# Kernel tuning notes

Hardware: AMD Instinct MI355X
Metric: run time of the kernel (lower is better)

Reference implementation:

```python
import jax, jax.numpy as jnp
import numpy as np

B, N, C = 2, 120000, 80
K = 300            # fixed NMS candidate pad per class (>> expected ~150 above threshold)
MAX_DET = 100      # max_detections_per_images
SCORE_THRES = 0.99875
NMS_THRES = 0.5
MIN_SIZE = 1e-3    # remove_small_boxes min_size
BBOX_CLIP = float(np.log(1000.0 / 16.0))  # standard decode clamp on dw, dh


def _decode(deltas, anchors):
    # activ_2_bbox: standard anchor-delta decode (xyxy anchors)
    wa = anchors[:, 2] - anchors[:, 0]
    ha = anchors[:, 3] - anchors[:, 1]
    cxa = anchors[:, 0] + 0.5 * wa
    cya = anchors[:, 1] + 0.5 * ha
    dx, dy = deltas[:, 0], deltas[:, 1]
    dw = jnp.minimum(deltas[:, 2], BBOX_CLIP)
    dh = jnp.minimum(deltas[:, 3], BBOX_CLIP)
    cx = dx * wa + cxa
    cy = dy * ha + cya
    w = jnp.exp(dw) * wa
    h = jnp.exp(dh) * ha
    return jnp.stack([cx - 0.5 * w, cy - 0.5 * h, cx + 0.5 * w, cy + 0.5 * h], axis=-1)


def _pairwise_iou(b):
    area = (b[:, 2] - b[:, 0]) * (b[:, 3] - b[:, 1])
    lt = jnp.maximum(b[:, None, :2], b[None, :, :2])
    rb = jnp.minimum(b[:, None, 2:], b[None, :, 2:])
    wh = jnp.clip(rb - lt, 0.0)
    inter = wh[..., 0] * wh[..., 1]
    return inter / (area[:, None] + area[None, :] - inter + 1e-9)


def _nms_keep(boxes, valid):
    # boxes sorted by descending score; greedy suppression over K candidates
    iou = jax.lax.stop_gradient(_pairwise_iou(boxes))  # masks only -> no grad path
    idx = jnp.arange(boxes.shape[0])
    def body(keep, i):
        suppress = keep[i] & (iou[i] > NMS_THRES) & (idx > i)
        return keep & ~suppress, None
    keep, _ = jax.lax.scan(body, valid, idx)
    return keep


def _per_image(box_pred, cls_pred, anchors, H, W):
    boxes = _decode(box_pred, anchors)
    boxes = jnp.stack([
        jnp.clip(boxes[:, 0], 0.0, W), jnp.clip(boxes[:, 1], 0.0, H),
        jnp.clip(boxes[:, 2], 0.0, W), jnp.clip(boxes[:, 3], 0.0, H)], axis=-1)
    big = ((boxes[:, 2] - boxes[:, 0]) >= MIN_SIZE) & ((boxes[:, 3] - boxes[:, 1]) >= MIN_SIZE)

    def class_step(valid, c):
        # faithful to the original: the validity set carries over across classes
        sc = cls_pred[:, c]
        v = valid & big & (sc > SCORE_THRES)
        ms = jnp.where(v, sc, -jnp.inf)
        sk, idx = jax.lax.top_k(ms, K)            # sorted desc, fixed-size pad
        vk = sk > -jnp.inf
        bk = boxes[idx]                            # [K,4]
        keep = _nms_keep(bk, vk)
        keep = keep & ((jnp.cumsum(keep) - 1) < MAX_DET)  # keep[:max_det]
        new_valid = jnp.zeros_like(valid).at[idx].set(keep)
        bk = jnp.where(keep[:, None], bk, 0.0)
        sk = jnp.where(keep, sk, 0.0)
        return new_valid, (bk, sk, keep)

    _, (bks, sks, keeps) = jax.lax.scan(class_step, jnp.ones(boxes.shape[0], bool), jnp.arange(C))
    out5 = jnp.concatenate([bks, sks[..., None]], axis=-1).reshape(C * K, 5)
    labels = jnp.broadcast_to(jnp.arange(C, dtype=jnp.int32)[:, None], (C, K)).reshape(C * K)
    return out5, labels, keeps.reshape(C * K)


def setup_inputs() -> dict:
    key = jax.random.key(0)
    k1, k2, k3, k4, k5 = jax.random.split(key, 5)
    H, W = 800, 1216
    box_preds = 0.2 * jax.random.normal(k1, (B, N, 4), jnp.float32)
    cls_preds = jax.random.uniform(k2, (B, N, C), dtype=jnp.float32)
    cx = jax.random.uniform(k3, (N,), dtype=jnp.float32) * W
    cy = jax.random.uniform(k4, (N,), dtype=jnp.float32) * H
    wh = 16.0 + 240.0 * jax.random.uniform(k5, (N, 2), dtype=jnp.float32)
    anchors = jnp.stack([cx - 0.5 * wh[:, 0], cy - 0.5 * wh[:, 1],
                         cx + 0.5 * wh[:, 0], cy + 0.5 * wh[:, 1]], axis=-1)
    return {"box_preds": box_preds, "cls_preds": cls_preds, "anchors": anchors,
            "image_h": H, "image_w": W}


def reference(box_preds, cls_preds, anchors, image_h, image_w):
    H = jnp.float32(image_h)
    W = jnp.float32(image_w)
    out5, labels, keep = jax.vmap(lambda bp, cp: _per_image(bp, cp, anchors, H, W))(box_preds, cls_preds)
    # out5: [B, C*K, 5] (x1,y1,x2,y2,score), zero-padded where keep is False
    return out5, labels, keep
```

## Files before the change

kernel.cpp:

```cpp
#include <hip/hip_runtime.h>
#include <stdint.h>

#define B_ 2
#define N_ 120000
#define C_ 80
#define K_ 300
#define MAXDET 100
#define CAP 1024
#define KTOP 300
#define NW 5

__device__ __constant__ float SCORE_THRES_F = 0.99875f;
__device__ __constant__ float NMS_THRES_F   = 0.5f;
__device__ __constant__ float MIN_SIZE_F    = 0.001f;
__device__ __constant__ float BBOX_CLIP_F   = 4.135166556742356f;

__global__ __launch_bounds__(256) void filter_init(
    const float* __restrict__ boxp, const float* __restrict__ clsp,
    const float* __restrict__ anch, const int* __restrict__ ih,
    const int* __restrict__ iw, int* __restrict__ counters,
    int* __restrict__ g_idx, float* __restrict__ g_sc,
    float4* __restrict__ g_bx, float* __restrict__ out) {
#pragma clang fp contract(off)
    const int NT  = gridDim.x * blockDim.x;
    const int tid = blockIdx.x * blockDim.x + threadIdx.x;

    const int CK  = C_ * K_;
    const int L0  = B_ * CK * 5;
    const int L1  = L0 + B_ * CK;
    const int TOT = L1 + B_ * CK;
    for (int i = tid; i < TOT; i += NT) {
        float v = 0.f;
        if (i >= L0 && i < L1) { int r = i - L0; v = (float)((r % CK) / K_); }
        out[i] = v;
    }

    const int BN = B_ * N_;
    float s[4]; int t4[4];
#pragma unroll
    for (int k = 0; k < 4; ++k) {
        int t = tid + k * NT;
        t4[k] = t;
        s[k] = (t < BN) ? clsp[(size_t)t * C_] : 0.f;
    }
#pragma unroll
    for (int k = 0; k < 4; ++k) {
        int t = t4[k];
        if (t < BN && s[k] > SCORE_THRES_F) {
            int b = t / N_, n = t - b * N_;
            float W = (float)iw[0], H = (float)ih[0];
            float4 d = *(const float4*)(boxp + (size_t)t * 4);
            float4 a = *(const float4*)(anch + (size_t)n * 4);
            float wa = a.z - a.x, ha = a.w - a.y;
            float cxa = a.x + 0.5f * wa, cya = a.y + 0.5f * ha;
            float dw = fminf(d.z, BBOX_CLIP_F), dh = fminf(d.w, BBOX_CLIP_F);
            float cx = d.x * wa + cxa, cy = d.y * ha + cya;
            float w = expf(dw) * wa, h = expf(dh) * ha;
            float x1 = cx - 0.5f * w, y1 = cy - 0.5f * h;
            float x2 = cx + 0.5f * w, y2 = cy + 0.5f * h;
            x1 = fminf(fmaxf(x1, 0.f), W);
            y1 = fminf(fmaxf(y1, 0.f), H);
            x2 = fminf(fmaxf(x2, 0.f), W);
            y2 = fminf(fmaxf(y2, 0.f), H);
            if ((x2 - x1 >= MIN_SIZE_F) && (y2 - y1 >= MIN_SIZE_F)) {
                int p = atomicAdd(&counters[b], 1);
                if (p < CAP) {
                    int q = b * CAP + p;
                    g_idx[q] = n;
                    g_sc[q]  = s[k];
                    g_bx[q]  = make_float4(x1, y1, x2, y2);
                }
            }
        }
    }
}

__global__ __launch_bounds__(256) void seq_nms(const float* __restrict__ clsp,
                                               const int* __restrict__ counters,
                                               const int* __restrict__ g_idx,
                                               const float* __restrict__ g_sc,
                                               const float4* __restrict__ g_bx,
                                               float* __restrict__ out) {
#pragma clang fp contract(off)
    const int b   = blockIdx.x;
    const int tid = threadIdx.x;
    const int BS  = blockDim.x;

    __shared__ __align__(16) float s_sc[CAP];
    __shared__ __align__(16) int   s_id[CAP];
    __shared__ float4 s_bx[CAP];
    __shared__ float  o_sc[KTOP];
    __shared__ int    o_id[KTOP];
    __shared__ float  o_ar[KTOP];
    __shared__ float  o_nsc[KTOP];
    __shared__ float4 o_bx[KTOP];
    __shared__ unsigned long long suppW[KTOP * NW];
    __shared__ unsigned long long keepm[NW];
    __shared__ int s_cnt, s_nk;
    __shared__ int    n_id[MAXDET];
    __shared__ float  n_sc[MAXDET];
    __shared__ float4 n_bx[MAXDET];

    if (tid == 0) s_nk = 0;
    const size_t CK = (size_t)C_ * K_;

    for (int c = 0; c < C_; ++c) {
        if (c > 0 && s_nk == 0) break;
        if (tid == 0) s_cnt = 0;
        __syncthreads();

        int m_in;
        if (c == 0) {
            int g = min(counters[b], CAP);
            for (int t = tid; t < g; t += BS) {
                int q = b * CAP + t;
                s_sc[t] = g_sc[q]; s_id[t] = g_idx[q]; s_bx[t] = g_bx[q];
            }
            __syncthreads();
            m_in = g;
        } else {
            int nk = s_nk;
            for (int t = tid; t < nk; t += BS) {
                float sv = n_sc[t];
                if (sv > SCORE_THRES_F) {
                    int p = atomicAdd(&s_cnt, 1);
                    s_sc[p] = sv; s_id[p] = n_id[t]; s_bx[p] = n_bx[t];
                }
            }
            __syncthreads();
            m_in = s_cnt;
        }
        int m = min(m_in, KTOP);
        if (m == 0) {
            if (tid == 0) s_nk = 0;
            __syncthreads();
            continue;
        }

        for (int i = tid; i < m_in; i += BS) {
            float si = s_sc[i]; int di = s_id[i]; float4 bx = s_bx[i];
            float ns = 0.f;
            if (c + 1 < C_) ns = clsp[((size_t)(b * N_) + di) * C_ + (c + 1)];
            int rank = 0;
            int m4 = m_in & ~3;
            for (int j = 0; j < m4; j += 4) {
                float4 sj = *(const float4*)&s_sc[j];
                int4   dj = *(const int4*)&s_id[j];
                rank += (sj.x > si) || (sj.x == si && dj.x < di);
                rank += (sj.y > si) || (sj.y == si && dj.y < di);
                rank += (sj.z > si) || (sj.z == si && dj.z < di);
                rank += (sj.w > si) || (sj.w == si && dj.w < di);
            }
            for (int j = m4; j < m_in; ++j) {
                float sj = s_sc[j];
                rank += (sj > si) || (sj == si && s_id[j] < di);
            }
            if (rank < KTOP) {
                o_sc[rank] = si; o_id[rank] = di; o_bx[rank] = bx;
                o_ar[rank] = (bx.z - bx.x) * (bx.w - bx.y);
                o_nsc[rank] = ns;
            }
        }
        __syncthreads();

        for (int i = tid; i < m; i += BS) {
            float4 bi = o_bx[i]; float ai = o_ar[i];
            for (int w = 0; w < NW; ++w) {
                unsigned long long msk = 0ull;
                int jlo = max(i + 1, w * 64);
                int jhi = min(m, w * 64 + 64);
#pragma unroll 4
                for (int j = jlo; j < jhi; ++j) {
                    float4 bj = o_bx[j];
                    float lx = fmaxf(bi.x, bj.x), ly = fmaxf(bi.y, bj.y);
                    float rx = fminf(bi.z, bj.z), ry = fminf(bi.w, bj.w);
                    float ww = fmaxf(rx - lx, 0.f), hh = fmaxf(ry - ly, 0.f);
                    float inter = ww * hh;
                    float arj = (bj.z - bj.x) * (bj.w - bj.y);
                    float iou = inter / (ai + arj - inter + 1e-9f);
                    if (iou > NMS_THRES_F) msk |= 1ull << (j & 63);
                }
                suppW[i * NW + w] = msk;
            }
        }
        __syncthreads();

        if (tid < 64) {
            int lane = tid;
            unsigned long long km = 0ull;
            if (lane < NW) {
                int nb = m - lane * 64;
                if (nb >= 64) km = ~0ull;
                else if (nb > 0) km = (1ull << nb) - 1ull;
            }
            unsigned long long srow = (lane < NW) ? suppW[lane] : 0ull;
            for (int i = 0; i < m; ++i) {
                unsigned long long nxt =
                    (lane < NW && i + 1 < m) ? suppW[(i + 1) * NW + lane] : 0ull;
                unsigned long long wv = __shfl(km, i >> 6);
                if ((wv >> (i & 63)) & 1ull) km &= ~srow;
                srow = nxt;
            }
            unsigned long long w0 = __shfl(km, 0), w1 = __shfl(km, 1),
                               w2 = __shfl(km, 2), w3 = __shfl(km, 3),
                               w4 = __shfl(km, 4);
            if (lane == 0) {
                unsigned long long arr[NW] = {w0, w1, w2, w3, w4};
                int cnt = 0;
                for (int w = 0; w < NW; ++w) {
                    unsigned long long x = arr[w];
                    if (cnt >= MAXDET) { arr[w] = 0ull; continue; }
                    int pc = __popcll(x);
                    if (cnt + pc > MAXDET) {
                        int need = MAXDET - cnt;
                        unsigned long long y = x;
                        for (int k2 = 0; k2 < need; ++k2) y &= y - 1ull;
                        arr[w] = x ^ y;
                        cnt = MAXDET;
                    } else cnt += pc;
                }
                int tot = 0;
                for (int w = 0; w < NW; ++w) { keepm[w] = arr[w]; tot += __popcll(arr[w]); }
                s_nk = tot;
            }
        }
        __syncthreads();

        for (int r = tid; r < m; r += BS) {
            unsigned long long wv = keepm[r >> 6];
            if ((wv >> (r & 63)) & 1ull) {
                int pos = __popcll(wv & ((1ull << (r & 63)) - 1ull));
                for (int w = 0; w < (r >> 6); ++w) pos += __popcll(keepm[w]);
                size_t row = (size_t)b * CK + (size_t)c * K_ + r;
                float4 bx = o_bx[r];
                float* o5 = out + row * 5;
                o5[0] = bx.x; o5[1] = bx.y; o5[2] = bx.z; o5[3] = bx.w;
                o5[4] = o_sc[r];
                out[(size_t)B_ * CK * 6 + row] = 1.0f;
                n_id[pos] = o_id[r];
                n_bx[pos] = bx;
                n_sc[pos] = o_nsc[r];
            }
        }
    }
}

extern "C" void kernel_launch(void* const* d_in, const int* in_sizes, int n_in,
                              void* d_out, int out_size, void* d_ws, size_t ws_size,
                              hipStream_t stream) {
    const float* boxp = (const float*)d_in[0];
    const float* clsp = (const float*)d_in[1];
    const float* anch = (const float*)d_in[2];
    const int*   ih   = (const int*)d_in[3];
    const int*   iw   = (const int*)d_in[4];
    float* out = (float*)d_out;

    int*    counters = (int*)d_ws;
    int*    g_idx = (int*)((char*)d_ws + 64);
    float*  g_sc  = (float*)((char*)d_ws + 64 + (size_t)B_ * CAP * 4);
    float4* g_bx  = (float4*)((char*)d_ws + 64 + (size_t)B_ * CAP * 8);

    hipMemsetAsync(d_ws, 0, 64, stream);
    filter_init<<<235, 256, 0, stream>>>(boxp, clsp, anch, ih, iw,
                                         counters, g_idx, g_sc, g_bx, out);
    seq_nms<<<B_, 256, 0, stream>>>(clsp, counters, g_idx, g_sc, g_bx, out);
}
```

Baseline: 153.0 us.

## Replace global atomic compaction with per-block slots and drop memset

The filter kernel now counts survivors with per-block shared-memory atomics and writes them into fixed per-block slot regions, storing per-block counts instead of bumping a global counter. The NMS kernel does a block-wide prefix scan over those counts to gather candidates into shared memory. This removes the hipMemsetAsync launch and contention on global atomics, and the score loads are issued before the output-zeroing loop so they overlap with it. The cost is that each block holds at most 32 candidates, so a denser input would silently drop boxes, and the gather in the NMS kernel is done serially per thread.

Result: faster. 149.8 us (-2.1%).

```diff
diff --git a/kernel.cpp b/kernel.cpp
--- a/kernel.cpp
+++ b/kernel.cpp
@@ -9,21 +9,37 @@
 #define CAP 1024
 #define KTOP 300
 #define NW 5
+#define NB 235
+#define TPB 256
+#define SLOTS 32
 
 __device__ __constant__ float SCORE_THRES_F = 0.99875f;
 __device__ __constant__ float NMS_THRES_F   = 0.5f;
 __device__ __constant__ float MIN_SIZE_F    = 0.001f;
 __device__ __constant__ float BBOX_CLIP_F   = 4.135166556742356f;
 
-__global__ __launch_bounds__(256) void filter_init(
+__global__ __launch_bounds__(TPB) void filter_init(
     const float* __restrict__ boxp, const float* __restrict__ clsp,
     const float* __restrict__ anch, const int* __restrict__ ih,
-    const int* __restrict__ iw, int* __restrict__ counters,
+    const int* __restrict__ iw, int* __restrict__ cnt,
     int* __restrict__ g_idx, float* __restrict__ g_sc,
     float4* __restrict__ g_bx, float* __restrict__ out) {
 #pragma clang fp contract(off)
-    const int NT  = gridDim.x * blockDim.x;
-    const int tid = blockIdx.x * blockDim.x + threadIdx.x;
+    __shared__ int lcnt[2];
+    const int blk = blockIdx.x;
+    const int ltid = threadIdx.x;
+    const int NT  = NB * TPB;
+    const int tid = blk * TPB + ltid;
+    if (ltid < 2) lcnt[ltid] = 0;
+
+    const int BN = B_ * N_;
+    float s[4]; int t4[4];
+#pragma unroll
+    for (int k = 0; k < 4; ++k) {
+        int t = tid + k * NT;
+        t4[k] = t;
+        s[k] = (t < BN) ? clsp[(size_t)t * C_] : 0.f;
+    }
 
     const int CK  = C_ * K_;
     const int L0  = B_ * CK * 5;
@@ -34,15 +50,8 @@
         if (i >= L0 && i < L1) { int r = i - L0; v = (float)((r % CK) / K_); }
         out[i] = v;
     }
-
-    const int BN = B_ * N_;
-    float s[4]; int t4[4];
-#pragma unroll
-    for (int k = 0; k < 4; ++k) {
-        int t = tid + k * NT;
-        t4[k] = t;
-        s[k] = (t < BN) ? clsp[(size_t)t * C_] : 0.f;
-    }
+    __syncthreads();
+
 #pragma unroll
     for (int k = 0; k < 4; ++k) {
         int t = t4[k];
@@ -63,9 +72,9 @@
             x2 = fminf(fmaxf(x2, 0.f), W);
             y2 = fminf(fmaxf(y2, 0.f), H);
             if ((x2 - x1 >= MIN_SIZE_F) && (y2 - y1 >= MIN_SIZE_F)) {
-                int p = atomicAdd(&counters[b], 1);
-                if (p < CAP) {
-                    int q = b * CAP + p;
+                int p = atomicAdd(&lcnt[b], 1);
+                if (p < SLOTS) {
+                    int q = (b * NB + blk) * SLOTS + p;
                     g_idx[q] = n;
                     g_sc[q]  = s[k];
                     g_bx[q]  = make_float4(x1, y1, x2, y2);
@@ -73,10 +82,12 @@
             }
         }
     }
+    __syncthreads();
+    if (ltid < 2) cnt[ltid * NB + blk] = min(lcnt[ltid], SLOTS);
 }
 
-__global__ __launch_bounds__(256) void seq_nms(const float* __restrict__ clsp,
-                                               const int* __restrict__ counters,
+__global__ __launch_bounds__(TPB) void seq_nms(const float* __restrict__ clsp,
+                                               const int* __restrict__ cnt,
                                                const int* __restrict__ g_idx,
                                                const float* __restrict__ g_sc,
                                                const float4* __restrict__ g_bx,
@@ -96,7 +107,8 @@
     __shared__ float4 o_bx[KTOP];
     __shared__ unsigned long long suppW[KTOP * NW];
     __shared__ unsigned long long keepm[NW];
-    __shared__ int s_cnt, s_nk;
+    __shared__ int s_cnt, s_nk, s_m;
+    __shared__ int wsum[4];
     __shared__ int    n_id[MAXDET];
     __shared__ float  n_sc[MAXDET];
     __shared__ float4 n_bx[MAXDET];
@@ -111,13 +123,30 @@
 
         int m_in;
         if (c == 0) {
-            int g = min(counters[b], CAP);
-            for (int t = tid; t < g; t += BS) {
-                int q = b * CAP + t;
-                s_sc[t] = g_sc[q]; s_id[t] = g_idx[q]; s_bx[t] = g_bx[q];
-            }
-            __syncthreads();
-            m_in = g;
+            int lane = tid & 63, wvi = tid >> 6;
+            int v = (tid < NB) ? cnt[b * NB + tid] : 0;
+            int x = v;
+            for (int d = 1; d < 64; d <<= 1) {
+                int y = __shfl_up(x, d);
+                if (lane >= d) x += y;
+            }
+            if (lane == 63) wsum[wvi] = x;
+            __syncthreads();
+            int offbase = 0;
+            for (int w = 0; w < wvi; ++w) offbase += wsum[w];
+            if (tid == BS - 1) s_m = offbase + x;
+            int excl = offbase + x - v;
+            for (int j = 0; j < v; ++j) {
+                int dst = excl + j;
+                if (dst < CAP) {
+                    int src = (b * NB + tid) * SLOTS + j;
+                    s_sc[dst] = g_sc[src];
+                    s_id[dst] = g_idx[src];
+                    s_bx[dst] = g_bx[src];
+                }
+            }
+            __syncthreads();
+            m_in = min(s_m, CAP);
         } else {
             int nk = s_nk;
             for (int t = tid; t < nk; t += BS) {
@@ -206,18 +235,18 @@
                                w4 = __shfl(km, 4);
             if (lane == 0) {
                 unsigned long long arr[NW] = {w0, w1, w2, w3, w4};
-                int cnt = 0;
+                int cnt2 = 0;
                 for (int w = 0; w < NW; ++w) {
                     unsigned long long x = arr[w];
-                    if (cnt >= MAXDET) { arr[w] = 0ull; continue; }
+                    if (cnt2 >= MAXDET) { arr[w] = 0ull; continue; }
                     int pc = __popcll(x);
-                    if (cnt + pc > MAXDET) {
-                        int need = MAXDET - cnt;
+                    if (cnt2 + pc > MAXDET) {
+                        int need = MAXDET - cnt2;
                         unsigned long long y = x;
                         for (int k2 = 0; k2 < need; ++k2) y &= y - 1ull;
                         arr[w] = x ^ y;
-                        cnt = MAXDET;
-                    } else cnt += pc;
+                        cnt2 = MAXDET;
+                    } else cnt2 += pc;
                 }
                 int tot = 0;
                 for (int w = 0; w < NW; ++w) { keepm[w] = arr[w]; tot += __popcll(arr[w]); }
@@ -255,13 +284,12 @@
     const int*   iw   = (const int*)d_in[4];
     float* out = (float*)d_out;
 
-    int*    counters = (int*)d_ws;
-    int*    g_idx = (int*)((char*)d_ws + 64);
-    float*  g_sc  = (float*)((char*)d_ws + 64 + (size_t)B_ * CAP * 4);
-    float4* g_bx  = (float4*)((char*)d_ws + 64 + (size_t)B_ * CAP * 8);
-
-    hipMemsetAsync(d_ws, 0, 64, stream);
-    filter_init<<<235, 256, 0, stream>>>(boxp, clsp, anch, ih, iw,
-                                         counters, g_idx, g_sc, g_bx, out);
-    seq_nms<<<B_, 256, 0, stream>>>(clsp, counters, g_idx, g_sc, g_bx, out);
+    int*    cnt   = (int*)d_ws;
+    int*    g_idx = (int*)((char*)d_ws + 4096);
+    float*  g_sc  = (float*)((char*)d_ws + 4096 + (size_t)B_ * NB * SLOTS * 4);
+    float4* g_bx  = (float4*)((char*)d_ws + 4096 + (size_t)B_ * NB * SLOTS * 8);
+
+    filter_init<<<NB, TPB, 0, stream>>>(boxp, clsp, anch, ih, iw,
+                                        cnt, g_idx, g_sc, g_bx, out);
+    seq_nms<<<B_, TPB, 0, stream>>>(clsp, cnt, g_idx, g_sc, g_bx, out);
 }
```
